# Kernel tuning notes

Measured on AMD Instinct MI355X. Metric: run time of the kernel, lower is better.

Reference implementation:

```python
import jax, jax.numpy as jnp
import numpy as np
from jax import lax

STATE_SIZE = 80
HIDDEN = 512
NC = 1
H = W = 32
STEPS = 64  # steps_range=(64,64)
THRESH = 0.01


def _maxpool3(x):
    # MaxPool2d(3, stride=1, padding=1) on NCHW
    return lax.reduce_window(x, -jnp.inf, lax.max, (1, 1, 3, 3), (1, 1, 1, 1), 'SAME')


def _conv3x3(x, w, b):
    y = lax.conv_general_dilated(x, w, (1, 1), 'SAME',
                                 dimension_numbers=('NCHW', 'OIHW', 'NCHW'))
    return y + b[None, :, None, None]


def _conv1x1(x, w, b):
    # w: (O, I, 1, 1) -> pointwise einsum
    return jnp.einsum('oi,bihw->bohw', w[:, :, 0, 0], x) + b[None, :, None, None]


def setup_inputs() -> dict:
    key = jax.random.key(0)
    ks = jax.random.split(key, 7)
    z = jax.random.normal(ks[0], (8, 100, 1, 1), dtype=jnp.float32)
    W1 = jax.random.normal(ks[1], (HIDDEN, STATE_SIZE, 3, 3), jnp.float32) / np.sqrt(STATE_SIZE * 9)
    b1 = jax.random.normal(ks[2], (HIDDEN,), jnp.float32) * 0.01
    W2 = jax.random.normal(ks[3], (HIDDEN, HIDDEN, 1, 1), jnp.float32) / np.sqrt(HIDDEN)
    b2 = jax.random.normal(ks[4], (HIDDEN,), jnp.float32) * 0.01
    # original code zero-inits the last conv; use small random weights so grads flow
    W3 = jax.random.normal(ks[5], (STATE_SIZE, HIDDEN, 1, 1), jnp.float32) * (0.01 / np.sqrt(HIDDEN))
    b3 = jax.random.normal(ks[6], (STATE_SIZE,), jnp.float32) * 0.001
    return {'z': z, 'W1': W1, 'b1': b1, 'W2': W2, 'b2': b2, 'W3': W3, 'b3': b3}


def _forward(z, W1, b1, W2, b2, W3, b3):
    N = z.shape[0]
    cH, cW = H // 2, W // 2
    state = jnp.zeros((N, STATE_SIZE, H, W), dtype=z.dtype)
    init_hidden = z[:, :STATE_SIZE - 1, 0, 0]  # (N, 79)
    state = state.at[:, 1:, cH, cW].set(init_hidden)
    state = state.at[:, 0, cH, cW].set(1.0)

    keys = jax.random.split(jax.random.key(42), STEPS)

    def ca_step(state, step_key):
        pre_living = _maxpool3(state[:, 0:1]) > THRESH
        perception = _conv3x3(state, W1, b1)
        h = jax.nn.relu(_conv1x1(perception, W2, b2))
        updates = _conv1x1(h, W3, b3)
        # stochastic update with p=1 (rand < 1 is always True, kept for fidelity)
        mask = jax.random.uniform(step_key, (state.shape[0], 1, H, W)) < 1.0
        state = state + mask.astype(state.dtype) * updates
        post_living = _maxpool3(state[:, 0:1]) > THRESH
        living = (post_living & pre_living).astype(state.dtype)
        return state * living, None

    state, _ = lax.scan(ca_step, state, keys)
    return state[:, :NC]  # (N, 1, H, W)


def reference(z, W1, b1, W2, b2, W3, b3):
    return _forward(z, W1, b1, W2, b2, W3, b3)
```

## Files before the change

### kernel.cpp

```cpp
#include <hip/hip_runtime.h>


#define NPIX 8192
#define T_ALIVE 0.01f

typedef _Float16 f16;
typedef __attribute__((ext_vector_type(8)))  _Float16 h8_t;
typedef __attribute__((ext_vector_type(4)))  _Float16 h4_t;
typedef __attribute__((ext_vector_type(16))) float    fx16;

__global__ __launch_bounds__(256) void tr512(
    const float* __restrict__ W2, float* __restrict__ W2T)
{
    __shared__ float t[32][33];
    const int bx = blockIdx.x & 15, by = blockIdx.x >> 4;
    const int x = threadIdx.x & 31, y8 = threadIdx.x >> 5;
#pragma unroll
    for (int r = 0; r < 32; r += 8)
        t[r + y8][x] = W2[(size_t)(by * 32 + r + y8) * 512 + bx * 32 + x];
    __syncthreads();
#pragma unroll
    for (int r = 0; r < 32; r += 8)
        W2T[(size_t)(bx * 32 + r + y8) * 512 + by * 32 + x] = t[x][r + y8];
}

__global__ __launch_bounds__(256) void wc32(
    const float* __restrict__ W2T, const float* __restrict__ W1,
    float* __restrict__ Wc)
{
    __shared__ float As[16][32];
    __shared__ float Bs[16][32];
    const int tid = threadIdx.x;
    const int ty = tid >> 3, tx = tid & 7;
    const int m0 = blockIdx.y * 32, n0 = blockIdx.x * 32;
    float acc[4] = {0.f, 0.f, 0.f, 0.f};

    for (int k0 = 0; k0 < 512; k0 += 16) {
#pragma unroll
        for (int t = 0; t < 2; ++t) {
            const int idx = tid + t * 256;
            const int r = idx >> 5, c = idx & 31;
            As[r][c] = W2T[(size_t)(k0 + r) * 512 + m0 + c];
            const int n = n0 + c;
            Bs[r][c] = (n < 720) ? W1[(size_t)(k0 + r) * 720 + n] : 0.f;
        }
        __syncthreads();
#pragma unroll
        for (int kk = 0; kk < 16; ++kk) {
            const float a = As[kk][ty];
#pragma unroll
            for (int j = 0; j < 4; ++j)
                acc[j] = fmaf(a, Bs[kk][tx * 4 + j], acc[j]);
        }
        __syncthreads();
    }
    const int m = m0 + ty;
#pragma unroll
    for (int j = 0; j < 4; ++j) {
        const int n = n0 + tx * 4 + j;
        if (n < 720) Wc[(size_t)m * 720 + n] = acc[j];
    }
}

__global__ __launch_bounds__(256) void bc_k(
    const float* __restrict__ W2, const float* __restrict__ b1,
    const float* __restrict__ b2, float* __restrict__ bc)
{
    const int m = blockIdx.x * 256 + threadIdx.x;
    if (m >= 512) return;
    float a = b2[m];
    for (int h = 0; h < 512; ++h) a += W2[m * 512 + h] * b1[h];
    bc[m] = a;
}

__global__ __launch_bounds__(256) void swz_wc2(
    const float* __restrict__ Wc, f16* __restrict__ Wcsw2)
{
    const int idx = blockIdx.x * 256 + threadIdx.x;
    if (idx >= 45 * 16 * 64) return;
    const int lane = idx & 63;
    const int t = idx >> 6;
    const int mtg = t & 15, ks = t >> 4;
    const int m = mtg * 32 + (lane & 31);
    const int k0 = ks * 16 + (lane >> 5) * 8;
    h8_t v;
#pragma unroll
    for (int j = 0; j < 8; ++j) {
        const int kp = k0 + j;
        const int tap = kp / 80, ci = kp - tap * 80;
        v[j] = (f16)Wc[(size_t)m * 720 + ci * 9 + tap];
    }
    *(h8_t*)(Wcsw2 + (size_t)idx * 8) = v;
}

__global__ __launch_bounds__(256) void swz_w32(
    const float* __restrict__ W3, f16* __restrict__ W3sw2)
{
    const int idx = blockIdx.x * 256 + threadIdx.x;
    if (idx >= 32 * 3 * 64) return;
    const int lane = idx & 63;
    const int t = idx >> 6;
    const int mt = t % 3, ks2 = t / 3;
    const int m = mt * 32 + (lane & 31);
    const int k0 = ks2 * 16 + (lane >> 5) * 8;
    h8_t v;
#pragma unroll
    for (int j = 0; j < 8; ++j)
        v[j] = (f16)((m < 80) ? W3[(size_t)m * 512 + k0 + j] : 0.f);
    *(h8_t*)(W3sw2 + (size_t)idx * 8) = v;
}

__global__ __launch_bounds__(256) void seed_k(
    const float* __restrict__ z, float* __restrict__ Sf32,
    f16* __restrict__ Smf16)
{
    const int idx = blockIdx.x * 256 + threadIdx.x;
    if (idx >= 640) return;
    const int b = idx / 80, c = idx - b * 80;
    const int n = b * 1024 + 16 * 32 + 16;
    const float v = (c == 0) ? 1.f : z[b * 100 + (c - 1)];
    Sf32[(size_t)c * NPIX + n] = v;
    Smf16[(size_t)n * 80 + c] = (f16)v;
}

__global__ __launch_bounds__(256) void aseed_init(
    const float* __restrict__ b3, float* __restrict__ Aseed)
{
    const int idx = blockIdx.x * 256 + threadIdx.x;
    if (idx >= NPIX) return;
    Aseed[idx] = b3[0] + (((idx & 1023) == 528) ? 1.f : 0.f);
}

__global__ __launch_bounds__(256) void k1_gemmH(
    const f16* __restrict__ Smf16, const f16* __restrict__ Wcsw2,
    const float* __restrict__ bc, const float* __restrict__ W3,
    f16* __restrict__ H, float* __restrict__ Aseed)
{
    __shared__ f16  msT[16320];
    __shared__ float bcL[64];
    __shared__ float waL[64];

    const int tid = threadIdx.x;
    const int lane = tid & 63, w = tid >> 6;
    const int li = lane & 31, q2 = lane >> 5;
    const int pb = blockIdx.x, mb = blockIdx.y;
    const int b = pb >> 3, y0 = (pb & 7) * 4;
    const int gb = b * 1024;

    if (tid < 64) {
        bcL[tid] = bc[mb * 64 + tid];
        waL[tid] = W3[mb * 64 + tid];
    }
    for (int idx = tid; idx < 2040; idx += 256) {
        const int p = idx / 10, cc = idx - p * 10;
        const int r = p / 34, xi = p - r * 34;
        const int gx = xi - 1, y = y0 - 1 + r;
        h8_t v;
        if (((unsigned)y < 32u) & ((unsigned)gx < 32u)) {
            v = *(const h8_t*)(Smf16 + (size_t)(gb + y * 32 + gx) * 80 + cc * 8);
        } else {
#pragma unroll
            for (int j = 0; j < 8; ++j) v[j] = (f16)0.f;
        }
        *(h8_t*)(msT + (size_t)(cc * 204 + p) * 8) = v;
    }
    __syncthreads();

    int pxh[9];
#pragma unroll
    for (int t = 0; t < 9; ++t)
        pxh[t] = ((t / 3) * 34 + li + (t % 3)) * 8;
    const int wbase = w * 272;

    fx16 acc[2];
#pragma unroll
    for (int i = 0; i < 2; ++i)
#pragma unroll
        for (int r = 0; r < 16; ++r) acc[i][r] = 0.f;

    h8_t abuf[8][2];
#pragma unroll
    for (int pk = 0; pk < 8; ++pk)
#pragma unroll
        for (int i = 0; i < 2; ++i)
            abuf[pk][i] = *(const h8_t*)(Wcsw2 +
                (((size_t)pk * 16 + (mb * 2 + i)) * 64 + lane) * 8);

#pragma unroll
    for (int ks = 0; ks < 45; ++ks) {
        const int o0 = 2 * ks, o1 = 2 * ks + 1;
        const int a0 = (o0 % 10) * 1632 + wbase + pxh[o0 / 10];
        const int a1 = (o1 % 10) * 1632 + wbase + pxh[o1 / 10];
        const h8_t bf = *(const h8_t*)(msT + (q2 ? a1 : a0));
        h8_t av[2];
#pragma unroll
        for (int i = 0; i < 2; ++i) av[i] = abuf[ks & 7][i];
        if (ks + 8 < 45) {
#pragma unroll
            for (int i = 0; i < 2; ++i)
                abuf[ks & 7][i] = *(const h8_t*)(Wcsw2 +
                    (((size_t)(ks + 8) * 16 + (mb * 2 + i)) * 64 + lane) * 8);
        }
#pragma unroll
        for (int i = 0; i < 2; ++i)
            acc[i] = __builtin_amdgcn_mfma_f32_32x32x16_f16(
                av[i], bf, acc[i], 0, 0, 0);
    }

    const size_t px = (size_t)(gb + (y0 + w) * 32 + li);
    float pd = 0.f;
#pragma unroll
    for (int i = 0; i < 2; ++i) {
#pragma unroll
        for (int aa = 0; aa < 4; ++aa) {
            const int chl = i * 32 + 8 * aa + 4 * q2;
            const int co = mb * 8 + i * 4 + aa;
            h4_t v4;
#pragma unroll
            for (int rb = 0; rb < 4; ++rb) {
                const float hv = fmaxf(acc[i][aa * 4 + rb] + bcL[chl + rb], 0.f);
                v4[rb] = (f16)hv;
                pd = fmaf(hv, waL[chl + rb], pd);
            }
            *(h4_t*)(H + ((size_t)co * NPIX + px) * 8 + 4 * q2) = v4;
        }
    }
    const float pd2 = __shfl_down(pd, 32);
    if (lane < 32) atomicAdd(&Aseed[px], pd + pd2);
}

__global__ __launch_bounds__(256) void k2_update(
    const f16* __restrict__ H, const f16* __restrict__ W3sw2,
    const float* __restrict__ b3,
    const float* __restrict__ Sold, float* __restrict__ Snew,
    f16* __restrict__ Smf16,
    const float* __restrict__ AseedC, float* __restrict__ AseedN)
{
    __shared__ float redT[12288];
    __shared__ float alphaO3[96];
    __shared__ float alphaN3[96];
    __shared__ float b3L[80];
    __shared__ float livef[32];

    const int tid = threadIdx.x;
    const int lane = tid & 63, w = tid >> 6;
    const int li = lane & 31, q2 = lane >> 5;
    const int blk = blockIdx.x;
    const int b = blk >> 5, y = blk & 31;
    const int gb = b * 1024;
    const size_t px = (size_t)(gb + y * 32 + li);

    h8_t hb[8], w3r[8][3];
#pragma unroll
    for (int k2 = 0; k2 < 8; ++k2) {
        const int ks2 = w * 8 + k2;
        hb[k2] = *(const h8_t*)(H + ((size_t)(ks2 * 2 + q2) * NPIX + px) * 8);
#pragma unroll
        for (int mt = 0; mt < 3; ++mt)
            w3r[k2][mt] = *(const h8_t*)(W3sw2 +
                (((size_t)ks2 * 3 + mt) * 64 + lane) * 8);
    }

    if (tid < 80) b3L[tid] = b3[tid];
    if (tid < 96) {
        const int r = tid >> 5, x = tid & 31, yy = y - 1 + r;
        const bool inb = (unsigned)yy < 32u;
        alphaO3[tid] = inb ? Sold[gb + yy * 32 + x]   : -1e30f;
        alphaN3[tid] = inb ? AseedC[gb + yy * 32 + x] : -1e30f;
    }

    fx16 acc3[3];
#pragma unroll
    for (int mt = 0; mt < 3; ++mt)
#pragma unroll
        for (int r = 0; r < 16; ++r) acc3[mt][r] = 0.f;
#pragma unroll
    for (int k2 = 0; k2 < 8; ++k2) {
#pragma unroll
        for (int mt = 0; mt < 3; ++mt)
            acc3[mt] = __builtin_amdgcn_mfma_f32_32x32x16_f16(
                w3r[k2][mt], hb[k2], acc3[mt], 0, 0, 0);
    }

#pragma unroll
    for (int mt = 0; mt < 3; ++mt)
#pragma unroll
        for (int aa = 0; aa < 4; ++aa) {
            float4 v;
            v.x = acc3[mt][aa * 4 + 0]; v.y = acc3[mt][aa * 4 + 1];
            v.z = acc3[mt][aa * 4 + 2]; v.w = acc3[mt][aa * 4 + 3];
            *(float4*)(redT + (((w * 3 + mt) * 4 + aa) * 256 + lane * 4)) = v;
        }
    __syncthreads();

    if (tid < 32) {
        float mN = -1e30f, mO = -1e30f;
#pragma unroll
        for (int r = 0; r < 3; ++r)
#pragma unroll
            for (int dx = -1; dx <= 1; ++dx) {
                const int xx = tid + dx;
                if ((unsigned)xx < 32u) {
                    mN = fmaxf(mN, alphaN3[r * 32 + xx]);
                    mO = fmaxf(mO, alphaO3[r * 32 + xx]);
                }
            }
        livef[tid] = (mN > T_ALIVE && mO > T_ALIVE) ? 1.f : 0.f;
    }
    __syncthreads();

    if (w < 3) {
        const int mt = w;
        const float lv = livef[li];
#pragma unroll
        for (int aa = 0; aa < 4; ++aa) {
            const float4 s0 = *(float4*)(redT + (((0 * 3 + mt) * 4 + aa) * 256 + lane * 4));
            const float4 s1 = *(float4*)(redT + (((1 * 3 + mt) * 4 + aa) * 256 + lane * 4));
            const float4 s2 = *(float4*)(redT + (((2 * 3 + mt) * 4 + aa) * 256 + lane * 4));
            const float4 s3 = *(float4*)(redT + (((3 * 3 + mt) * 4 + aa) * 256 + lane * 4));
            const float t4[4] = {s0.x + s1.x + s2.x + s3.x,
                                 s0.y + s1.y + s2.y + s3.y,
                                 s0.z + s1.z + s2.z + s3.z,
                                 s0.w + s1.w + s2.w + s3.w};
            const int ch0 = mt * 32 + 8 * aa + 4 * q2;
            if (ch0 + 3 < 80) {
                h4_t v4;
                float vrb0 = 0.f;
#pragma unroll
                for (int rb = 0; rb < 4; ++rb) {
                    const int ch = ch0 + rb;
                    const size_t idx = (size_t)ch * NPIX + px;
                    const float v = (Sold[idx] + t4[rb] + b3L[ch]) * lv;
                    Snew[idx] = v;
                    v4[rb] = (f16)v;
                    if (rb == 0) vrb0 = v;
                }
                *(h4_t*)(Smf16 + px * 80 + ch0) = v4;
                if (mt == 0 && aa == 0 && q2 == 0)
                    AseedN[px] = vrb0 + b3L[0];
            }
        }
    }
}

extern "C" void kernel_launch(void* const* d_in, const int* in_sizes, int n_in,
                              void* d_out, int out_size, void* d_ws, size_t ws_size,
                              hipStream_t stream)
{
    const float* z  = (const float*)d_in[0];
    const float* W1 = (const float*)d_in[1];
    const float* b1 = (const float*)d_in[2];
    const float* W2 = (const float*)d_in[3];
    const float* b2 = (const float*)d_in[4];
    const float* W3 = (const float*)d_in[5];
    const float* b3 = (const float*)d_in[6];

    char* ws = (char*)d_ws;
    float* S0    = (float*)ws;  ws += (size_t)80 * NPIX * 4;
    float* S1    = (float*)ws;  ws += (size_t)80 * NPIX * 4;
    f16*   Sm0   = (f16*)ws;   ws += (size_t)NPIX * 80 * 2;
    f16*   Sm1   = (f16*)ws;   ws += (size_t)NPIX * 80 * 2;
    float* As0   = (float*)ws;  ws += NPIX * 4;
    float* As1   = (float*)ws;  ws += NPIX * 4;
    float* bc    = (float*)ws;  ws += 512 * 4;
    float* Wc    = (float*)ws;  ws += (size_t)512 * 720 * 4;
    float* W2T   = (float*)ws;  ws += (size_t)512 * 512 * 4;
    f16*   Wcsw2 = (f16*)ws;   ws += (size_t)45 * 16 * 64 * 8 * 2;
    f16*   W3sw2 = (f16*)ws;   ws += (size_t)32 * 3 * 64 * 8 * 2;
    f16*   H     = (f16*)ws;   ws += (size_t)64 * NPIX * 8 * 2;

    hipMemsetAsync(S0, 0, (size_t)80 * NPIX * 4, stream);
    hipMemsetAsync(Sm0, 0, (size_t)NPIX * 80 * 2, stream);
    seed_k<<<3, 256, 0, stream>>>(z, S0, Sm0);
    aseed_init<<<32, 256, 0, stream>>>(b3, As0);
    tr512<<<256, 256, 0, stream>>>(W2, W2T);
    wc32<<<dim3(23, 16), 256, 0, stream>>>(W2T, W1, Wc);
    bc_k<<<2, 256, 0, stream>>>(W2, b1, b2, bc);
    swz_wc2<<<180, 256, 0, stream>>>(Wc, Wcsw2);
    swz_w32<<<24, 256, 0, stream>>>(W3, W3sw2);

    float* Scur = S0;  float* Snxt = S1;
    f16*   Mcur = Sm0; f16*   Mnxt = Sm1;
    for (int s = 0; s < 64; ++s) {
        float* AsC = (s & 1) ? As1 : As0;
        float* AsN = (s & 1) ? As0 : As1;
        k1_gemmH<<<dim3(64, 8), 256, 0, stream>>>(Mcur, Wcsw2, bc, W3, H, AsC);
        k2_update<<<256, 256, 0, stream>>>(H, W3sw2, b3, Scur, Snxt, Mnxt,
                                           AsC, AsN);
        float* t = Scur; Scur = Snxt; Snxt = t;
        f16*   m = Mcur; Mcur = Mnxt; Mnxt = m;
    }

    hipMemcpyAsync(d_out, Scur, NPIX * sizeof(float),
                   hipMemcpyDeviceToDevice, stream);
}
```

Baseline: 1.398 ms.

## Enlarge k1 tiles to 8 rows with 512 threads and batch halo loads

Each k1_gemmH block now covers 8 image rows with 8 waves (512 threads) instead of 4 rows with 4 waves. This lowers the halo overhead in the shared-memory state tile and halves the number of blocks that reload the same weight fragments. The tile load is split into a register-staged gather followed by LDS stores, so more global loads are in flight at once. The aseed_init launch is merged into seed_k. The cost is fewer blocks (256) for the GPU, larger LDS use per block and higher register pressure.

```diff
diff --git a/kernel.cpp b/kernel.cpp
--- a/kernel.cpp
+++ b/kernel.cpp
@@ -111,10 +111,13 @@
 }
 
 __global__ __launch_bounds__(256) void seed_k(
-    const float* __restrict__ z, float* __restrict__ Sf32,
-    f16* __restrict__ Smf16)
+    const float* __restrict__ z, const float* __restrict__ b3,
+    float* __restrict__ Sf32, f16* __restrict__ Smf16,
+    float* __restrict__ Aseed)
 {
     const int idx = blockIdx.x * 256 + threadIdx.x;
+    if (idx < NPIX)
+        Aseed[idx] = b3[0] + (((idx & 1023) == 528) ? 1.f : 0.f);
     if (idx >= 640) return;
     const int b = idx / 80, c = idx - b * 80;
     const int n = b * 1024 + 16 * 32 + 16;
@@ -123,20 +126,12 @@
     Smf16[(size_t)n * 80 + c] = (f16)v;
 }
 
-__global__ __launch_bounds__(256) void aseed_init(
-    const float* __restrict__ b3, float* __restrict__ Aseed)
-{
-    const int idx = blockIdx.x * 256 + threadIdx.x;
-    if (idx >= NPIX) return;
-    Aseed[idx] = b3[0] + (((idx & 1023) == 528) ? 1.f : 0.f);
-}
-
-__global__ __launch_bounds__(256) void k1_gemmH(
+__global__ __launch_bounds__(512) void k1_gemmH(
     const f16* __restrict__ Smf16, const f16* __restrict__ Wcsw2,
     const float* __restrict__ bc, const float* __restrict__ W3,
     f16* __restrict__ H, float* __restrict__ Aseed)
 {
-    __shared__ f16  msT[16320];
+    __shared__ f16  msT[27200];
     __shared__ float bcL[64];
     __shared__ float waL[64];
 
@@ -144,25 +139,37 @@
     const int lane = tid & 63, w = tid >> 6;
     const int li = lane & 31, q2 = lane >> 5;
     const int pb = blockIdx.x, mb = blockIdx.y;
-    const int b = pb >> 3, y0 = (pb & 7) * 4;
+    const int b = pb >> 2, y0 = (pb & 3) * 8;
     const int gb = b * 1024;
 
     if (tid < 64) {
         bcL[tid] = bc[mb * 64 + tid];
         waL[tid] = W3[mb * 64 + tid];
     }
-    for (int idx = tid; idx < 2040; idx += 256) {
-        const int p = idx / 10, cc = idx - p * 10;
-        const int r = p / 34, xi = p - r * 34;
-        const int gx = xi - 1, y = y0 - 1 + r;
-        h8_t v;
-        if (((unsigned)y < 32u) & ((unsigned)gx < 32u)) {
-            v = *(const h8_t*)(Smf16 + (size_t)(gb + y * 32 + gx) * 80 + cc * 8);
-        } else {
-#pragma unroll
-            for (int j = 0; j < 8; ++j) v[j] = (f16)0.f;
-        }
-        *(h8_t*)(msT + (size_t)(cc * 204 + p) * 8) = v;
+    h8_t sv[7];
+#pragma unroll
+    for (int t = 0; t < 7; ++t) {
+        const int idx = tid + t * 512;
+        if (idx < 3400) {
+            const int p = idx / 10, cc = idx - p * 10;
+            const int r = p / 34, xi = p - r * 34;
+            const int gx = xi - 1, y = y0 - 1 + r;
+            if (((unsigned)y < 32u) & ((unsigned)gx < 32u)) {
+                sv[t] = *(const h8_t*)(Smf16 +
+                         (size_t)(gb + y * 32 + gx) * 80 + cc * 8);
+            } else {
+#pragma unroll
+                for (int j = 0; j < 8; ++j) sv[t][j] = (f16)0.f;
+            }
+        }
+    }
+#pragma unroll
+    for (int t = 0; t < 7; ++t) {
+        const int idx = tid + t * 512;
+        if (idx < 3400) {
+            const int p = idx / 10, cc = idx - p * 10;
+            *(h8_t*)(msT + (size_t)(cc * 340 + p) * 8) = sv[t];
+        }
     }
     __syncthreads();
 
@@ -189,8 +196,8 @@
 #pragma unroll
     for (int ks = 0; ks < 45; ++ks) {
         const int o0 = 2 * ks, o1 = 2 * ks + 1;
-        const int a0 = (o0 % 10) * 1632 + wbase + pxh[o0 / 10];
-        const int a1 = (o1 % 10) * 1632 + wbase + pxh[o1 / 10];
+        const int a0 = (o0 % 10) * 2720 + wbase + pxh[o0 / 10];
+        const int a1 = (o1 % 10) * 2720 + wbase + pxh[o1 / 10];
         const h8_t bf = *(const h8_t*)(msT + (q2 ? a1 : a0));
         h8_t av[2];
 #pragma unroll
@@ -371,8 +378,7 @@
 
     hipMemsetAsync(S0, 0, (size_t)80 * NPIX * 4, stream);
     hipMemsetAsync(Sm0, 0, (size_t)NPIX * 80 * 2, stream);
-    seed_k<<<3, 256, 0, stream>>>(z, S0, Sm0);
-    aseed_init<<<32, 256, 0, stream>>>(b3, As0);
+    seed_k<<<32, 256, 0, stream>>>(z, b3, S0, Sm0, As0);
     tr512<<<256, 256, 0, stream>>>(W2, W2T);
     wc32<<<dim3(23, 16), 256, 0, stream>>>(W2T, W1, Wc);
     bc_k<<<2, 256, 0, stream>>>(W2, b1, b2, bc);
@@ -384,7 +390,7 @@
     for (int s = 0; s < 64; ++s) {
         float* AsC = (s & 1) ? As1 : As0;
         float* AsN = (s & 1) ? As0 : As1;
-        k1_gemmH<<<dim3(64, 8), 256, 0, stream>>>(Mcur, Wcsw2, bc, W3, H, AsC);
+        k1_gemmH<<<dim3(32, 8), 512, 0, stream>>>(Mcur, Wcsw2, bc, W3, H, AsC);
         k2_update<<<256, 256, 0, stream>>>(H, W3sw2, b3, Scur, Snxt, Mnxt,
                                            AsC, AsN);
         float* t = Scur; Scur = Snxt; Snxt = t;
```

Result: slower. 1.464 ms (+4.7%).
